# Optimization experiments

Measured on AMD Instinct MI355X. Metric: run time of the kernel, lower is better.

The kernel has to match this reference:

```python
import jax, jax.numpy as jnp
import numpy as np

B, N, SEQ = 4, 1024, 512
FOUR = SEQ // 2 + 1           # 257, rfft output length
E = N * 32                    # edges from adjacency nonzeros
H1, C1 = 3, 10                # gat1: heads=3, out=10 (concat -> 30)
H2, C2 = 1, 1                 # gat2: heads=1, out=1
NEG_SLOPE = 0.2               # GATConv default negative_slope
PRE_L = 1


def setup_inputs() -> dict:
    ks = jax.random.split(jax.random.key(0), 14)
    occ = jax.random.normal(ks[0], (B, N, SEQ), dtype=jnp.float32)
    prc = jax.random.normal(ks[1], (B, N, SEQ), dtype=jnp.float32)
    # edge_index = adj_dense.nonzero().t(): indices in [0, N)
    edge_index = jax.random.randint(ks[2], (2, E), 0, N, dtype=jnp.int32)
    s = 0.3
    W1 = jax.random.normal(ks[3], (2, H1 * C1), dtype=jnp.float32) * s
    att_src1 = jax.random.normal(ks[4], (1, H1, C1), dtype=jnp.float32) * s
    att_dst1 = jax.random.normal(ks[5], (1, H1, C1), dtype=jnp.float32) * s
    b1 = jnp.zeros((H1 * C1,), dtype=jnp.float32)
    W2 = jax.random.normal(ks[6], (H1 * C1, H2 * C2), dtype=jnp.float32) * s
    att_src2 = jax.random.normal(ks[7], (1, H2, C2), dtype=jnp.float32) * s
    att_dst2 = jax.random.normal(ks[8], (1, H2, C2), dtype=jnp.float32) * s
    b2 = jnp.zeros((H2 * C2,), dtype=jnp.float32)
    dec_W = jax.random.normal(ks[9], (FOUR, PRE_L), dtype=jnp.float32) * (1.0 / np.sqrt(FOUR))
    dec_b = jnp.zeros((PRE_L,), dtype=jnp.float32)
    return {"occ": occ, "prc": prc, "edge_index": edge_index,
            "W1": W1, "att_src1": att_src1, "att_dst1": att_dst1, "b1": b1,
            "W2": W2, "att_src2": att_src2, "att_dst2": att_dst2, "b2": b2,
            "dec_W": dec_W, "dec_b": dec_b}


def gat_layer(x, src, dst, W, att_src, att_dst, bias, heads, ch):
    # x: [Nt, Fin]. PyG GATConv (concat=True, eval mode: no dropout).
    Nt = x.shape[0]
    h = (x @ W).reshape(Nt, heads, ch)                 # [Nt, H, C]
    a_src = jnp.sum(h * att_src, axis=-1)              # [Nt, H]
    a_dst = jnp.sum(h * att_dst, axis=-1)              # [Nt, H]
    e = jax.nn.leaky_relu(a_src[src] + a_dst[dst], NEG_SLOPE)  # [Ee, H]
    # segment softmax over destination nodes
    m = jax.ops.segment_max(e, dst, num_segments=Nt)   # [Nt, H]
    ex = jnp.exp(e - m[dst])
    denom = jax.ops.segment_sum(ex, dst, num_segments=Nt)
    alpha = ex / denom[dst]                            # [Ee, H]
    out = jax.ops.segment_sum(h[src] * alpha[..., None], dst, num_segments=Nt)
    return out.reshape(Nt, heads * ch) + bias


def reference(occ, prc, edge_index, W1, att_src1, att_dst1, b1,
              W2, att_src2, att_dst2, b2, dec_W, dec_b):
    # stack -> [B, N, SEQ, 2]; rfft over seq dim; keep real part
    x = jnp.stack([occ, prc], axis=-1)
    x = jnp.fft.rfft(x, axis=2).real                   # [B, N, FOUR, 2]
    x = x.reshape(-1, 2)                               # [Nt, 2], Nt = B*N*FOUR
    Nt = x.shape[0]
    # GATConv adds self-loops for every row of x (num_nodes = Nt)
    loops = jnp.arange(Nt, dtype=edge_index.dtype)
    src = jnp.concatenate([edge_index[0], loops])
    dst = jnp.concatenate([edge_index[1], loops])
    x = gat_layer(x, src, dst, W1, att_src1, att_dst1, b1, H1, C1)  # [Nt, 30]
    x = jax.nn.elu(x)
    x = gat_layer(x, src, dst, W2, att_src2, att_dst2, b2, H2, C2)  # [Nt, 1]
    # dropout is identity in eval mode
    x = x.reshape(B, N, FOUR)
    return x @ dec_W + dec_b                           # [B, N, PRE_L]
```

## Files before the change

### kernel.cpp

```cpp
#include <hip/hip_runtime.h>
#include <math.h>

constexpr int Bc    = 4;
constexpr int Nc    = 1024;
constexpr int SEQc  = 512;
constexpr int FOURc = 257;
constexpr int NROWS = Bc * Nc;
constexpr int NSMALL = 1024;
constexpr int F1c   = 30;
constexpr int PADH  = 32;
constexpr int CAP   = 128;
constexpr int XPAD  = 258;
constexpr float NEG_SLOPE = 0.2f;

#define DEVFN static __device__ __forceinline__

__global__ __launch_bounds__(256) void k_xf(
    const float* __restrict__ occ, const float* __restrict__ prc,
    float* __restrict__ xf, int* __restrict__ cnt) {
  __shared__ float4 z[2][128];
  __shared__ float sp[2][6];
  const int tid  = threadIdx.x;
  const int lane = tid & 63;
  const int wid  = tid >> 6;
  const int jrow = wid >> 1;
  const int half = wid & 1;
  const int row  = blockIdx.x * 2 + jrow;

  if (blockIdx.x == 0) {
#pragma unroll
    for (int j = 0; j < 4; ++j) cnt[tid + 256 * j] = 0;
  }

  {
    const int j = tid >> 7;
    const int t = tid & 127;
    const float* ro = occ + (size_t)(blockIdx.x * 2 + j) * SEQc;
    const float* rp = prc + (size_t)(blockIdx.x * 2 + j) * SEQc;
    if (t == 0) {
      sp[j][0] = ro[0];                 sp[j][1] = rp[0];
      sp[j][2] = ro[128] + ro[384];     sp[j][3] = rp[128] + rp[384];
      sp[j][4] = ro[256];               sp[j][5] = rp[256];
    } else {
      float ao = ro[t] + ro[SEQc - t];
      float bo = ro[256 - t] + ro[256 + t];
      float ap = rp[t] + rp[SEQc - t];
      float bp = rp[256 - t] + rp[256 + t];
      z[j][t] = make_float4(ao + bo, ap + bp, ao - bo, ap - bp);
    }
  }
  __syncthreads();

  const int k0 = half * 128 + 2 * lane;
  const float a = 6.283185307179586f / 512.0f;
  float ce = cosf((float)k0 * a),       cpe = 1.f, m2e = 2.f * ce;
  float co = cosf((float)(k0 + 1) * a), cpo = 1.f, m2o = 2.f * co;
  float aeo = 0.f, aep = 0.f, aoo = 0.f, aop = 0.f;

#pragma unroll 4
  for (int t = 1; t < 128; ++t) {
    float4 zv = z[jrow][t];
    aeo = fmaf(zv.x, ce, aeo);
    aep = fmaf(zv.y, ce, aep);
    aoo = fmaf(zv.z, co, aoo);
    aop = fmaf(zv.w, co, aop);
    float ne = fmaf(m2e, ce, -cpe); cpe = ce; ce = ne;
    float no = fmaf(m2o, co, -cpo); cpo = co; co = no;
  }

  const float y0o = sp[jrow][0], y0p = sp[jrow][1];
  const float y128o = sp[jrow][2], y128p = sp[jrow][3];
  const float x256o = sp[jrow][4], x256p = sp[jrow][5];
  const float s128 = (lane & 1) ? -1.f : 1.f;

  float4 st;
  st.x = aeo + y0o + s128 * y128o + x256o;
  st.y = aep + y0p + s128 * y128p + x256p;
  st.z = aoo + y0o - x256o;
  st.w = aop + y0p - x256p;
  *reinterpret_cast<float4*>(xf + ((size_t)row * XPAD + k0) * 2) = st;

  if (half == 0) {
    float sgn = (lane & 1) ? -1.f : 1.f;
    float4 zhi = z[jrow][lane + 64];
    float so = sgn * zhi.x, spp = sgn * zhi.y;
    if (lane >= 1) {
      float4 zlo = z[jrow][lane];
      so  = fmaf(sgn, zlo.x, so);
      spp = fmaf(sgn, zlo.y, spp);
    }
#pragma unroll
    for (int off = 32; off; off >>= 1) {
      so  += __shfl_xor(so, off);
      spp += __shfl_xor(spp, off);
    }
    if (lane == 0) {
      float2 st2;
      st2.x = y0o + y128o + so + x256o;
      st2.y = y0p + y128p + spp + x256p;
      *reinterpret_cast<float2*>(xf + ((size_t)row * XPAD + 256) * 2) = st2;
    }
  }
}

DEVFN float node_v(float xo, float xp,
                   const float* w1s, const float* b1s, const float* w2s, float b2v) {
  float s = 0.f;
#pragma unroll
  for (int jj = 0; jj < F1c; ++jj) {
    float h = fmaf(xo, w1s[jj], fmaf(xp, w1s[F1c + jj], b1s[jj]));
    float e = h > 0.f ? h : (__expf(h) - 1.f);
    s = fmaf(e, w2s[jj], s);
  }
  return s + b2v;
}

DEVFN void small_prep(int node, float xo, float xp,
                      const float* w1s, const float* s1, const float* d1,
                      float* h1s, float* a1s, float* a1d) {
#pragma unroll
  for (int h = 0; h < 3; ++h) {
    float as = 0.f, ad = 0.f;
#pragma unroll
    for (int c = 0; c < 10; ++c) {
      int jj = h * 10 + c;
      float hv = fmaf(xo, w1s[jj], xp * w1s[F1c + jj]);
      h1s[node * PADH + jj] = hv;
      as = fmaf(hv, s1[jj], as);
      ad = fmaf(hv, d1[jj], ad);
    }
    a1s[node * 4 + h] = as;
    a1d[node * 4 + h] = ad;
  }
}

__global__ __launch_bounds__(256) void k_post(
    const float* __restrict__ xf,
    const float* __restrict__ W1, const float* __restrict__ b1,
    const float* __restrict__ W2, const float* __restrict__ b2,
    const float* __restrict__ as1, const float* __restrict__ ad1,
    const float* __restrict__ decW, const float* __restrict__ decb,
    float* __restrict__ out, float* __restrict__ vsm,
    float* __restrict__ h1s, float* __restrict__ a1s, float* __restrict__ a1d,
    const int* __restrict__ ei, int E,
    int* __restrict__ cnt, int* __restrict__ srcs2) {
  const int tid = threadIdx.x;

  if (blockIdx.x >= NROWS) {
    const int base = (blockIdx.x - NROWS) * 256 + tid;
    const int tot  = E + NSMALL;
    for (int e = base; e < tot; e += 32 * 256) {
      int src, dst;
      if (e < E) { src = ei[e]; dst = ei[E + e]; }
      else       { src = dst = e - E; }
      int pos = atomicAdd(&cnt[dst], 1);
      if (pos < CAP) srcs2[dst * CAP + pos] = src;
    }
    return;
  }

  __shared__ float wl[192];
  __shared__ float red[4];
  const int row = blockIdx.x;
  if      (tid < 60)  wl[tid] = W1[tid];
  else if (tid < 90)  wl[tid] = b1[tid - 60];
  else if (tid < 120) wl[tid] = W2[tid - 90];
  else if (tid < 150) wl[tid] = as1[tid - 120];
  else if (tid < 180) wl[tid] = ad1[tid - 150];
  __syncthreads();
  const float* w1s = wl;
  const float* b1s = wl + 60;
  const float* w2s = wl + 90;
  const float* s1  = wl + 120;
  const float* d1  = wl + 150;
  const float b2v  = b2[0];
  const bool smallrow = (row < 4);

  float2 v2 = *reinterpret_cast<const float2*>(xf + ((size_t)row * XPAD + tid) * 2);
  float vv = node_v(v2.x, v2.y, w1s, b1s, w2s, b2v);
  float s = vv * decW[tid];
  if (tid == 0) {
    float2 v6 = *reinterpret_cast<const float2*>(xf + ((size_t)row * XPAD + 256) * 2);
    float v256 = node_v(v6.x, v6.y, w1s, b1s, w2s, b2v);
    s = fmaf(v256, decW[256], s);
    if (smallrow) {
      int node = row * FOURc + 256;
      if (node < NSMALL) {
        vsm[node] = v256;
        small_prep(node, v6.x, v6.y, w1s, s1, d1, h1s, a1s, a1d);
      }
    }
  }
  if (smallrow) {
    int node = row * FOURc + tid;
    if (node < NSMALL) {
      vsm[node] = vv;
      small_prep(node, v2.x, v2.y, w1s, s1, d1, h1s, a1s, a1d);
    }
  }
#pragma unroll
  for (int off = 32; off; off >>= 1) s += __shfl_xor(s, off);
  if ((tid & 63) == 0) red[tid >> 6] = s;
  __syncthreads();
  if (tid == 0) out[row] = red[0] + red[1] + red[2] + red[3] + decb[0];
}

__global__ __launch_bounds__(256) void k_g1(
    const int* __restrict__ cnt, const int* __restrict__ srcs2,
    const float* __restrict__ a1s, const float* __restrict__ a1d,
    const float* __restrict__ h1s,
    const float* __restrict__ b1, const float* __restrict__ W2,
    const float* __restrict__ as2, const float* __restrict__ ad2,
    float* __restrict__ h2s, float* __restrict__ a2s, float* __restrict__ a2d) {
  const int lane = threadIdx.x & 63;
  const int dst  = blockIdx.x * 4 + (threadIdx.x >> 6);
  const int deg  = cnt[dst];
  const int* sp  = srcs2 + dst * CAP;
  const float ad0 = a1d[dst * 4], ad1v = a1d[dst * 4 + 1], ad2v = a1d[dst * 4 + 2];
  float den[3] = {0.f, 0.f, 0.f};
  float num[F1c];
#pragma unroll
  for (int j = 0; j < F1c; ++j) num[j] = 0.f;

  for (int p = lane; p < deg; p += 64) {
    int src = sp[p];
    const float4* hs4 = reinterpret_cast<const float4*>(h1s + src * PADH);
    float4 av = *reinterpret_cast<const float4*>(a1s + src * 4);
    float x0 = av.x + ad0;
    float x1 = av.y + ad1v;
    float x2 = av.z + ad2v;
    x0 = x0 > 0.f ? x0 : NEG_SLOPE * x0;
    x1 = x1 > 0.f ? x1 : NEG_SLOPE * x1;
    x2 = x2 > 0.f ? x2 : NEG_SLOPE * x2;
    float ev[3] = {__expf(x0), __expf(x1), __expf(x2)};
    den[0] += ev[0]; den[1] += ev[1]; den[2] += ev[2];
#pragma unroll
    for (int m = 0; m < 7; ++m) {
      float4 hv = hs4[m];
      num[4 * m + 0] = fmaf(ev[(4 * m + 0) / 10], hv.x, num[4 * m + 0]);
      num[4 * m + 1] = fmaf(ev[(4 * m + 1) / 10], hv.y, num[4 * m + 1]);
      num[4 * m + 2] = fmaf(ev[(4 * m + 2) / 10], hv.z, num[4 * m + 2]);
      num[4 * m + 3] = fmaf(ev[(4 * m + 3) / 10], hv.w, num[4 * m + 3]);
    }
    float2 h7 = *reinterpret_cast<const float2*>(h1s + src * PADH + 28);
    num[28] = fmaf(ev[2], h7.x, num[28]);
    num[29] = fmaf(ev[2], h7.y, num[29]);
  }
#pragma unroll
  for (int h = 0; h < 3; ++h)
#pragma unroll
    for (int off = 32; off; off >>= 1) den[h] += __shfl_xor(den[h], off);
#pragma unroll
  for (int j = 0; j < F1c; ++j)
#pragma unroll
    for (int off = 32; off; off >>= 1) num[j] += __shfl_xor(num[j], off);

  if (lane == 0) {
    float h2 = 0.f;
#pragma unroll
    for (int jj = 0; jj < F1c; ++jj) {
      float x2 = num[jj] / den[jj / 10] + b1[jj];
      x2 = x2 > 0.f ? x2 : (__expf(x2) - 1.f);
      h2 = fmaf(x2, W2[jj], h2);
    }
    h2s[dst] = h2;
    a2s[dst] = h2 * as2[0];
    a2d[dst] = h2 * ad2[0];
  }
}

__global__ __launch_bounds__(256) void k_g2(
    const int* __restrict__ cnt, const int* __restrict__ srcs2,
    const float* __restrict__ a2s, const float* __restrict__ a2d,
    const float* __restrict__ h2s, const float* __restrict__ b2,
    const float* __restrict__ vsm, const float* __restrict__ decW,
    float* __restrict__ out) {
  __shared__ float rcor[4];
  __shared__ int   rrow[4];
  const int tid  = threadIdx.x;
  const int lane = tid & 63;
  const int wid  = tid >> 6;
  const int dst  = blockIdx.x * 4 + wid;
  const int deg  = cnt[dst];
  const int* sp  = srcs2 + dst * CAP;
  const float adv = a2d[dst];
  float den = 0.f, num = 0.f;
  for (int p = lane; p < deg; p += 64) {
    int src = sp[p];
    float x = a2s[src] + adv;
    x = x > 0.f ? x : NEG_SLOPE * x;
    float ex = __expf(x);
    den += ex;
    num = fmaf(ex, h2s[src], num);
  }
#pragma unroll
  for (int off = 32; off; off >>= 1) {
    den += __shfl_xor(den, off);
    num += __shfl_xor(num, off);
  }
  if (lane == 0) {
    float val2v = num / den + b2[0];
    int r = dst / FOURc;
    int k = dst - r * FOURc;
    rcor[wid] = (val2v - vsm[dst]) * decW[k];
    rrow[wid] = r;
  }
  __syncthreads();
  if (tid == 0) {
    float acc = rcor[0];
#pragma unroll
    for (int i = 1; i < 4; ++i) {
      if (rrow[i] == rrow[0]) acc += rcor[i];
      else atomicAdd(&out[rrow[i]], rcor[i]);
    }
    atomicAdd(&out[rrow[0]], acc);
  }
}

extern "C" void kernel_launch(void* const* d_in, const int* in_sizes, int n_in,
                              void* d_out, int out_size, void* d_ws, size_t ws_size,
                              hipStream_t stream) {
  const float* occ  = (const float*)d_in[0];
  const float* prc  = (const float*)d_in[1];
  const int*   ei   = (const int*)d_in[2];
  const float* W1   = (const float*)d_in[3];
  const float* as1  = (const float*)d_in[4];
  const float* ad1  = (const float*)d_in[5];
  const float* b1   = (const float*)d_in[6];
  const float* W2   = (const float*)d_in[7];
  const float* as2  = (const float*)d_in[8];
  const float* ad2  = (const float*)d_in[9];
  const float* b2   = (const float*)d_in[10];
  const float* decW = (const float*)d_in[11];
  const float* decb = (const float*)d_in[12];
  const int E = in_sizes[2] / 2;

  float* ws = (float*)d_ws;
  float* xf   = ws;
  float* h1s  = xf + (size_t)NROWS * XPAD * 2;
  float* a1s  = h1s + NSMALL * PADH;
  float* a1d  = a1s + NSMALL * 4;
  float* h2s  = a1d + NSMALL * 4;
  float* a2s  = h2s + NSMALL;
  float* a2d  = a2s + NSMALL;
  float* vsm  = a2d + NSMALL;
  int*   cnt  = (int*)(vsm + NSMALL);
  int*   srcs2 = cnt + NSMALL;

  k_xf<<<NROWS / 2, 256, 0, stream>>>(occ, prc, xf, cnt);

  k_post<<<NROWS + 32, 256, 0, stream>>>(xf, W1, b1, W2, b2, as1, ad1,
                                         decW, decb, (float*)d_out, vsm,
                                         h1s, a1s, a1d, ei, E, cnt, srcs2);

  k_g1<<<NSMALL / 4, 256, 0, stream>>>(cnt, srcs2, a1s, a1d, h1s,
                                       b1, W2, as2, ad2, h2s, a2s, a2d);
  k_g2<<<NSMALL / 4, 256, 0, stream>>>(cnt, srcs2, a2s, a2d, h2s, b2,
                                       vsm, decW, (float*)d_out);
}
```

Measured before the change: 54.16 us.

## Fuse post, GAT1 and GAT2 stages into one cooperative persistent kernel

Replaces the three launches k_post, k_g1 and k_g2 with a single cooperative kernel of 512 blocks. The blocks loop over the row and scatter work units, then the GAT1 and GAT2 destination work, with grid-wide syncs between stages. This removes per-launch overhead and the gaps between dependent kernels. It adds the cost of grid.sync and of a persistent-loop structure. The old three-kernel path is kept as a fallback if the cooperative launch fails.

```diff
diff --git a/kernel.cpp b/kernel.cpp
--- a/kernel.cpp
+++ b/kernel.cpp
@@ -1,5 +1,8 @@
 #include <hip/hip_runtime.h>
+#include <hip/hip_cooperative_groups.h>
 #include <math.h>
+
+namespace cg = cooperative_groups;
 
 constexpr int Bc    = 4;
 constexpr int Nc    = 1024;
@@ -134,48 +137,13 @@
   }
 }
 
-__global__ __launch_bounds__(256) void k_post(
-    const float* __restrict__ xf,
-    const float* __restrict__ W1, const float* __restrict__ b1,
-    const float* __restrict__ W2, const float* __restrict__ b2,
-    const float* __restrict__ as1, const float* __restrict__ ad1,
-    const float* __restrict__ decW, const float* __restrict__ decb,
-    float* __restrict__ out, float* __restrict__ vsm,
-    float* __restrict__ h1s, float* __restrict__ a1s, float* __restrict__ a1d,
-    const int* __restrict__ ei, int E,
-    int* __restrict__ cnt, int* __restrict__ srcs2) {
-  const int tid = threadIdx.x;
-
-  if (blockIdx.x >= NROWS) {
-    const int base = (blockIdx.x - NROWS) * 256 + tid;
-    const int tot  = E + NSMALL;
-    for (int e = base; e < tot; e += 32 * 256) {
-      int src, dst;
-      if (e < E) { src = ei[e]; dst = ei[E + e]; }
-      else       { src = dst = e - E; }
-      int pos = atomicAdd(&cnt[dst], 1);
-      if (pos < CAP) srcs2[dst * CAP + pos] = src;
-    }
-    return;
-  }
-
-  __shared__ float wl[192];
-  __shared__ float red[4];
-  const int row = blockIdx.x;
-  if      (tid < 60)  wl[tid] = W1[tid];
-  else if (tid < 90)  wl[tid] = b1[tid - 60];
-  else if (tid < 120) wl[tid] = W2[tid - 90];
-  else if (tid < 150) wl[tid] = as1[tid - 120];
-  else if (tid < 180) wl[tid] = ad1[tid - 150];
-  __syncthreads();
-  const float* w1s = wl;
-  const float* b1s = wl + 60;
-  const float* w2s = wl + 90;
-  const float* s1  = wl + 120;
-  const float* d1  = wl + 150;
-  const float b2v  = b2[0];
+DEVFN void post_row(int row, int tid, int lane, int wid,
+                    const float* xf, const float* w1s, const float* b1s,
+                    const float* w2s, const float* s1, const float* d1,
+                    float b2v, const float* decW, const float* decb,
+                    float* out, float* vsm, float* h1s, float* a1s, float* a1d,
+                    float* red) {
   const bool smallrow = (row < 4);
-
   float2 v2 = *reinterpret_cast<const float2*>(xf + ((size_t)row * XPAD + tid) * 2);
   float vv = node_v(v2.x, v2.y, w1s, b1s, w2s, b2v);
   float s = vv * decW[tid];
@@ -200,22 +168,33 @@
   }
 #pragma unroll
   for (int off = 32; off; off >>= 1) s += __shfl_xor(s, off);
-  if ((tid & 63) == 0) red[tid >> 6] = s;
+  if (lane == 0) red[wid] = s;
   __syncthreads();
   if (tid == 0) out[row] = red[0] + red[1] + red[2] + red[3] + decb[0];
-}
-
-__global__ __launch_bounds__(256) void k_g1(
-    const int* __restrict__ cnt, const int* __restrict__ srcs2,
-    const float* __restrict__ a1s, const float* __restrict__ a1d,
-    const float* __restrict__ h1s,
-    const float* __restrict__ b1, const float* __restrict__ W2,
-    const float* __restrict__ as2, const float* __restrict__ ad2,
-    float* __restrict__ h2s, float* __restrict__ a2s, float* __restrict__ a2d) {
-  const int lane = threadIdx.x & 63;
-  const int dst  = blockIdx.x * 4 + (threadIdx.x >> 6);
-  const int deg  = cnt[dst];
-  const int* sp  = srcs2 + dst * CAP;
+  __syncthreads();
+}
+
+DEVFN void scatter_chunk(int chunk, int tid, const int* ei, int E,
+                         int* cnt, int* srcs2) {
+  const int base = chunk * 256 + tid;
+  const int tot  = E + NSMALL;
+  for (int e = base; e < tot; e += 32 * 256) {
+    int src, dst;
+    if (e < E) { src = ei[e]; dst = ei[E + e]; }
+    else       { src = dst = e - E; }
+    int pos = atomicAdd(&cnt[dst], 1);
+    if (pos < CAP) srcs2[dst * CAP + pos] = src;
+  }
+}
+
+DEVFN void g1_dst(int dst, int lane,
+                  const int* cnt, const int* srcs2,
+                  const float* a1s, const float* a1d, const float* h1s,
+                  const float* b1s, const float* w2s,
+                  const float* as2, const float* ad2,
+                  float* h2s, float* a2s, float* a2d) {
+  const int deg = cnt[dst];
+  const int* sp = srcs2 + dst * CAP;
   const float ad0 = a1d[dst * 4], ad1v = a1d[dst * 4 + 1], ad2v = a1d[dst * 4 + 2];
   float den[3] = {0.f, 0.f, 0.f};
   float num[F1c];
@@ -259,9 +238,9 @@
     float h2 = 0.f;
 #pragma unroll
     for (int jj = 0; jj < F1c; ++jj) {
-      float x2 = num[jj] / den[jj / 10] + b1[jj];
+      float x2 = num[jj] / den[jj / 10] + b1s[jj];
       x2 = x2 > 0.f ? x2 : (__expf(x2) - 1.f);
-      h2 = fmaf(x2, W2[jj], h2);
+      h2 = fmaf(x2, w2s[jj], h2);
     }
     h2s[dst] = h2;
     a2s[dst] = h2 * as2[0];
@@ -269,20 +248,13 @@
   }
 }
 
-__global__ __launch_bounds__(256) void k_g2(
-    const int* __restrict__ cnt, const int* __restrict__ srcs2,
-    const float* __restrict__ a2s, const float* __restrict__ a2d,
-    const float* __restrict__ h2s, const float* __restrict__ b2,
-    const float* __restrict__ vsm, const float* __restrict__ decW,
-    float* __restrict__ out) {
-  __shared__ float rcor[4];
-  __shared__ int   rrow[4];
-  const int tid  = threadIdx.x;
-  const int lane = tid & 63;
-  const int wid  = tid >> 6;
-  const int dst  = blockIdx.x * 4 + wid;
-  const int deg  = cnt[dst];
-  const int* sp  = srcs2 + dst * CAP;
+DEVFN void g2_dst(int dst, int tid, int lane, int wid,
+                  const int* cnt, const int* srcs2,
+                  const float* a2s, const float* a2d, const float* h2s,
+                  float b2v, const float* vsm, const float* decW,
+                  float* out, float* rcor, int* rrow) {
+  const int deg = cnt[dst];
+  const int* sp = srcs2 + dst * CAP;
   const float adv = a2d[dst];
   float den = 0.f, num = 0.f;
   for (int p = lane; p < deg; p += 64) {
@@ -299,7 +271,7 @@
     num += __shfl_xor(num, off);
   }
   if (lane == 0) {
-    float val2v = num / den + b2[0];
+    float val2v = num / den + b2v;
     int r = dst / FOURc;
     int k = dst - r * FOURc;
     rcor[wid] = (val2v - vsm[dst]) * decW[k];
@@ -315,6 +287,112 @@
     }
     atomicAdd(&out[rrow[0]], acc);
   }
+}
+
+__global__ __launch_bounds__(256, 4) void k_coop(
+    const float* __restrict__ xf,
+    const float* __restrict__ W1, const float* __restrict__ b1,
+    const float* __restrict__ W2, const float* __restrict__ b2,
+    const float* __restrict__ as1, const float* __restrict__ ad1,
+    const float* __restrict__ as2, const float* __restrict__ ad2,
+    const float* __restrict__ decW, const float* __restrict__ decb,
+    const int* __restrict__ ei, int E,
+    float* __restrict__ out, float* __restrict__ vsm,
+    float* __restrict__ h1s, float* __restrict__ a1s, float* __restrict__ a1d,
+    float* __restrict__ h2s, float* __restrict__ a2s, float* __restrict__ a2d,
+    int* __restrict__ cnt, int* __restrict__ srcs2) {
+  cg::grid_group grid = cg::this_grid();
+  const int tid  = threadIdx.x;
+  const int lane = tid & 63;
+  const int wid  = tid >> 6;
+  const int nb   = gridDim.x;
+
+  __shared__ float wl[192];
+  __shared__ float red[4];
+  __shared__ float rcor[4];
+  __shared__ int   rrow[4];
+
+  if      (tid < 60)  wl[tid] = W1[tid];
+  else if (tid < 90)  wl[tid] = b1[tid - 60];
+  else if (tid < 120) wl[tid] = W2[tid - 90];
+  else if (tid < 150) wl[tid] = as1[tid - 120];
+  else if (tid < 180) wl[tid] = ad1[tid - 150];
+  __syncthreads();
+  const float* w1s = wl;
+  const float* b1s = wl + 60;
+  const float* w2s = wl + 90;
+  const float* s1  = wl + 120;
+  const float* d1  = wl + 150;
+  const float b2v  = b2[0];
+
+  for (int u = blockIdx.x; u < NROWS + 32; u += nb) {
+    if (u < NROWS)
+      post_row(u, tid, lane, wid, xf, w1s, b1s, w2s, s1, d1, b2v,
+               decW, decb, out, vsm, h1s, a1s, a1d, red);
+    else
+      scatter_chunk(u - NROWS, tid, ei, E, cnt, srcs2);
+  }
+  grid.sync();
+
+  for (int u = blockIdx.x; u < NSMALL / 4; u += nb)
+    g1_dst(u * 4 + wid, lane, cnt, srcs2, a1s, a1d, h1s,
+           b1s, w2s, as2, ad2, h2s, a2s, a2d);
+  grid.sync();
+
+  for (int u = blockIdx.x; u < NSMALL / 4; u += nb)
+    g2_dst(u * 4 + wid, tid, lane, wid, cnt, srcs2, a2s, a2d, h2s,
+           b2v, vsm, decW, out, rcor, rrow);
+}
+
+__global__ __launch_bounds__(256) void k_post(
+    const float* __restrict__ xf,
+    const float* __restrict__ W1, const float* __restrict__ b1,
+    const float* __restrict__ W2, const float* __restrict__ b2,
+    const float* __restrict__ as1, const float* __restrict__ ad1,
+    const float* __restrict__ decW, const float* __restrict__ decb,
+    float* __restrict__ out, float* __restrict__ vsm,
+    float* __restrict__ h1s, float* __restrict__ a1s, float* __restrict__ a1d,
+    const int* __restrict__ ei, int E,
+    int* __restrict__ cnt, int* __restrict__ srcs2) {
+  const int tid = threadIdx.x;
+  if (blockIdx.x >= NROWS) {
+    scatter_chunk(blockIdx.x - NROWS, tid, ei, E, cnt, srcs2);
+    return;
+  }
+  __shared__ float wl[192];
+  __shared__ float red[4];
+  if      (tid < 60)  wl[tid] = W1[tid];
+  else if (tid < 90)  wl[tid] = b1[tid - 60];
+  else if (tid < 120) wl[tid] = W2[tid - 90];
+  else if (tid < 150) wl[tid] = as1[tid - 120];
+  else if (tid < 180) wl[tid] = ad1[tid - 150];
+  __syncthreads();
+  post_row(blockIdx.x, tid, tid & 63, tid >> 6, xf, wl, wl + 60, wl + 90,
+           wl + 120, wl + 150, b2[0], decW, decb, out, vsm, h1s, a1s, a1d, red);
+}
+
+__global__ __launch_bounds__(256) void k_g1(
+    const int* __restrict__ cnt, const int* __restrict__ srcs2,
+    const float* __restrict__ a1s, const float* __restrict__ a1d,
+    const float* __restrict__ h1s,
+    const float* __restrict__ b1, const float* __restrict__ W2,
+    const float* __restrict__ as2, const float* __restrict__ ad2,
+    float* __restrict__ h2s, float* __restrict__ a2s, float* __restrict__ a2d) {
+  g1_dst(blockIdx.x * 4 + (threadIdx.x >> 6), threadIdx.x & 63,
+         cnt, srcs2, a1s, a1d, h1s, b1, W2, as2, ad2, h2s, a2s, a2d);
+}
+
+__global__ __launch_bounds__(256) void k_g2(
+    const int* __restrict__ cnt, const int* __restrict__ srcs2,
+    const float* __restrict__ a2s, const float* __restrict__ a2d,
+    const float* __restrict__ h2s, const float* __restrict__ b2,
+    const float* __restrict__ vsm, const float* __restrict__ decW,
+    float* __restrict__ out) {
+  __shared__ float rcor[4];
+  __shared__ int   rrow[4];
+  g2_dst(blockIdx.x * 4 + (threadIdx.x >> 6), threadIdx.x, threadIdx.x & 63,
+         threadIdx.x >> 6, cnt, srcs2, a2s, a2d, h2s, b2[0], vsm, decW,
+         out, rcor, rrow);
 }
 
 extern "C" void kernel_launch(void* const* d_in, const int* in_sizes, int n_in,
@@ -333,7 +411,7 @@
   const float* b2   = (const float*)d_in[10];
   const float* decW = (const float*)d_in[11];
   const float* decb = (const float*)d_in[12];
-  const int E = in_sizes[2] / 2;
+  int E = in_sizes[2] / 2;
 
   float* ws = (float*)d_ws;
   float* xf   = ws;
@@ -349,12 +427,23 @@
 
   k_xf<<<NROWS / 2, 256, 0, stream>>>(occ, prc, xf, cnt);
 
-  k_post<<<NROWS + 32, 256, 0, stream>>>(xf, W1, b1, W2, b2, as1, ad1,
-                                         decW, decb, (float*)d_out, vsm,
-                                         h1s, a1s, a1d, ei, E, cnt, srcs2);
-
-  k_g1<<<NSMALL / 4, 256, 0, stream>>>(cnt, srcs2, a1s, a1d, h1s,
-                                       b1, W2, as2, ad2, h2s, a2s, a2d);
-  k_g2<<<NSMALL / 4, 256, 0, stream>>>(cnt, srcs2, a2s, a2d, h2s, b2,
-                                       vsm, decW, (float*)d_out);
-}
+  float* outp = (float*)d_out;
+  void* args[] = {
+    (void*)&xf, (void*)&W1, (void*)&b1, (void*)&W2, (void*)&b2,
+    (void*)&as1, (void*)&ad1, (void*)&as2, (void*)&ad2,
+    (void*)&decW, (void*)&decb, (void*)&ei, (void*)&E,
+    (void*)&outp, (void*)&vsm, (void*)&h1s, (void*)&a1s, (void*)&a1d,
+    (void*)&h2s, (void*)&a2s, (void*)&a2d, (void*)&cnt, (void*)&srcs2
+  };
+  hipError_t err = hipLaunchCooperativeKernel(
+      reinterpret_cast<void*>(k_coop), dim3(512), dim3(256), args, 0, stream);
+  if (err != hipSuccess) {
+    k_post<<<NROWS + 32, 256, 0, stream>>>(xf, W1, b1, W2, b2, as1, ad1,
+                                           decW, decb, outp, vsm,
+                                           h1s, a1s, a1d, ei, E, cnt, srcs2);
+    k_g1<<<NSMALL / 4, 256, 0, stream>>>(cnt, srcs2, a1s, a1d, h1s,
+                                         b1, W2, as2, ad2, h2s, a2s, a2d);
+    k_g2<<<NSMALL / 4, 256, 0, stream>>>(cnt, srcs2, a2s, a2d, h2s, b2,
+                                         vsm, decW, outp);
+  }
+}
```

Result: slower. 184.5 us (+240.7%).
